# Kernel optimization log

Hardware: AMD Instinct MI355X
Metric: run time of the kernel (lower is better)

Reference implementation:

```python
import jax, jax.numpy as jnp
import numpy as np
import math

N, E = 50000, 800000
NFEAT, HID, NCLASS = 512, 96, 64
NUM_LAYERS = 8
ALPHA, THETA = 0.1, 0.5


def setup_inputs() -> dict:
    key = jax.random.key(0)
    ks = jax.random.split(key, 8)
    x = jax.random.normal(ks[0], (N, NFEAT), dtype=jnp.float32)
    # dense_to_sparse(adj_t) -> edge_index; weights are discarded by the module,
    # so propagation uses unit edge weights. We generate the edge list directly.
    edge_index = jax.random.randint(ks[1], (2, E), 0, N, dtype=jnp.int32)
    s_in = 1.0 / math.sqrt(NFEAT)
    s_hid = 1.0 / math.sqrt(HID)
    W_in = jax.random.uniform(ks[2], (NFEAT, HID), jnp.float32, -s_in, s_in)
    b_in = jax.random.uniform(ks[3], (HID,), jnp.float32, -s_in, s_in)
    conv_W = jax.random.uniform(ks[4], (NUM_LAYERS, HID, HID), jnp.float32, -s_hid, s_hid)
    W_out = jax.random.uniform(ks[5], (HID, NCLASS), jnp.float32, -s_hid, s_hid)
    b_out = jax.random.uniform(ks[6], (NCLASS,), jnp.float32, -s_hid, s_hid)
    return {"x": x, "edge_index": edge_index, "W_in": W_in, "b_in": b_in,
            "conv_W": conv_W, "W_out": W_out, "b_out": b_out}


def reference(x, edge_index, W_in, b_in, conv_W, W_out, b_out):
    # Eval mode: dropout is identity.
    src, dst = edge_index[0], edge_index[1]
    h = jax.nn.relu(x @ W_in + b_in)          # [N, HID]
    x0 = h
    for layer in range(NUM_LAYERS):
        beta = math.log(THETA / (layer + 1) + 1.0)
        # sparse propagation: out[i] = sum over edges (j -> i) of h[j]
        agg = jax.ops.segment_sum(h[src], dst, num_segments=N)   # [N, HID]
        hc = (1.0 - ALPHA) * agg + ALPHA * x0                    # initial residual
        h = jax.nn.relu((1.0 - beta) * hc + beta * (hc @ conv_W[layer]))
    out = h @ W_out + b_out                   # [N, NCLASS]
    return jax.nn.log_softmax(out, axis=-1)
```

## Files before the change

kernel.cpp:

```cpp
#include <hip/hip_runtime.h>
#include <math.h>

#define N_NODES 50000
#define N_EDGES 800000
#define NFEAT   512
#define HID     96
#define NCLASS  64
#define NUM_LAYERS 8
#define ALPHA   0.1f
#define NSB     49
#define NBB     196

typedef __attribute__((ext_vector_type(8))) short short8;
typedef __attribute__((ext_vector_type(4))) float f32x4;

__device__ __forceinline__ unsigned short f2bf(float f) {
    unsigned int u = __float_as_uint(f);
    unsigned int r = u + 0x7FFF + ((u >> 16) & 1);
    return (unsigned short)(r >> 16);
}
__device__ __forceinline__ float bflo(unsigned int u) { return __uint_as_float(u << 16); }
__device__ __forceinline__ float bfhi(unsigned int u) { return __uint_as_float(u & 0xFFFF0000u); }
__device__ __forceinline__ float bf2f(short s) {
    return __uint_as_float(((unsigned int)(unsigned short)s) << 16);
}

__global__ void hist_kernel(const int* __restrict__ dst, int* __restrict__ deg) {
    int e = blockIdx.x * blockDim.x + threadIdx.x;
    if (e < N_EDGES) atomicAdd(&deg[dst[e]], 1);
}

__global__ void scan1_kernel(const int* __restrict__ deg, int* __restrict__ row_start,
                             int* __restrict__ blk_sum) {
    __shared__ int sd[1024];
    int t = threadIdx.x;
    int i = blockIdx.x * 1024 + t;
    int v = (i < N_NODES) ? ((deg[i] + 3) & ~3) : 0;
    sd[t] = v;
    __syncthreads();
    for (int off = 1; off < 1024; off <<= 1) {
        int tv = (t >= off) ? sd[t - off] : 0;
        __syncthreads();
        sd[t] += tv;
        __syncthreads();
    }
    if (i < N_NODES) row_start[i] = sd[t] - v;
    if (t == 1023) blk_sum[blockIdx.x] = sd[1023];
}

__global__ void scan2_kernel(const int* __restrict__ blk_sum, int* __restrict__ blk_off) {
    if (threadIdx.x == 0) {
        int acc = 0;
        for (int b = 0; b < NSB; b++) { blk_off[b] = acc; acc += blk_sum[b]; }
    }
}

__global__ void scan3_kernel(int* __restrict__ row_start, const int* __restrict__ blk_off) {
    int i = blockIdx.x * 1024 + threadIdx.x;
    if (i < N_NODES) row_start[i] += blk_off[blockIdx.x];
}

__global__ void fill_kernel(const int* __restrict__ src, const int* __restrict__ dst,
                            const int* __restrict__ row_start, int* __restrict__ cursor,
                            int* __restrict__ csr_src) {
    int e = blockIdx.x * blockDim.x + threadIdx.x;
    if (e < N_EDGES) {
        int d = dst[e];
        int pos = row_start[d] + atomicAdd(&cursor[d], 1);
        csr_src[pos] = src[e];
    }
}

__global__ void pad_kernel(const int* __restrict__ deg, const int* __restrict__ row_start,
                           int* __restrict__ csr_src) {
    int n = blockIdx.x * blockDim.x + threadIdx.x;
    if (n < N_NODES) {
        int d = deg[n], pd = (d + 3) & ~3, rs = row_start[n];
        for (int p = d; p < pd; p++) csr_src[rs + p] = N_NODES;
    }
}

__global__ __launch_bounds__(256) void bin_hist2_kernel(
        const int* __restrict__ deg, int* __restrict__ node_rank,
        int* __restrict__ blk_bin_cnt) {
    __shared__ int lh[64];
    int t = threadIdx.x;
    if (t < 64) lh[t] = 0;
    __syncthreads();
    int n = blockIdx.x * 256 + t;
    if (n < N_NODES) {
        int nq = (deg[n] + 3) >> 2; if (nq > 63) nq = 63;
        node_rank[n] = atomicAdd(&lh[nq], 1);
    }
    __syncthreads();
    if (t < 64) blk_bin_cnt[blockIdx.x * 64 + t] = lh[t];
}

__global__ void bin_offsets_kernel(const int* __restrict__ blk_bin_cnt,
                                   int* __restrict__ blk_bin_off,
                                   int* __restrict__ bin_base) {
    __shared__ int tot[64];
    int b = threadIdx.x;
    int acc = 0;
    for (int blk = 0; blk < NBB; blk++) {
        blk_bin_off[blk * 64 + b] = acc;
        acc += blk_bin_cnt[blk * 64 + b];
    }
    tot[b] = acc;
    __syncthreads();
    if (b == 0) {
        int a = 0;
        for (int i = 63; i >= 0; i--) { bin_base[i] = a; a += tot[i]; }
    }
}

__global__ __launch_bounds__(256) void bin_place_kernel(
        const int* __restrict__ deg, const int* __restrict__ node_rank,
        const int* __restrict__ blk_bin_off, const int* __restrict__ bin_base,
        int* __restrict__ perm) {
    int n = blockIdx.x * 256 + threadIdx.x;
    if (n < N_NODES) {
        int nq = (deg[n] + 3) >> 2; if (nq > 63) nq = 63;
        perm[bin_base[nq] + blk_bin_off[blockIdx.x * 64 + nq] + node_rank[n]] = n;
    }
}

__global__ void zero_dummy_kernel(short* __restrict__ h0, short* __restrict__ hb,
                                  short* __restrict__ hc) {
    int t = threadIdx.x;
    if (t < HID) {
        h0[(size_t)N_NODES * HID + t] = 0;
        hb[(size_t)N_NODES * HID + t] = 0;
        hc[(size_t)N_NODES * HID + t] = 0;
    }
}

__global__ void convert_win_kernel(const float* __restrict__ W, short* __restrict__ Wt) {
    int n = blockIdx.x;
    int k = threadIdx.x;
    Wt[(size_t)n * NFEAT + k] = (short)f2bf(W[(size_t)k * HID + n]);
}

__global__ void convert_wout_kernel(const float* __restrict__ W, short* __restrict__ Wt) {
    int n = blockIdx.x;
    int k = threadIdx.x;
    Wt[(size_t)n * HID + k] = (short)f2bf(W[(size_t)k * NCLASS + n]);
}

__global__ void convert_wconv_kernel(const float* __restrict__ W, short* __restrict__ Wc) {
    int n = blockIdx.x;
    int l = blockIdx.y;
    int k = threadIdx.x;
    Wc[(size_t)l * HID * HID + (size_t)n * HID + k] =
        (short)f2bf(W[(size_t)l * HID * HID + (size_t)k * HID + n]);
}

__global__ __launch_bounds__(256) void gemm_in_kernel(
        const float* __restrict__ x, const short* __restrict__ Wt,
        const float* __restrict__ b, short* __restrict__ h0) {
    int tid  = threadIdx.x;
    int wave = tid >> 6, lane = tid & 63;
    int quad = lane >> 4, l16 = lane & 15;
    int row0 = blockIdx.x * 64 + wave * 16;
    int arow = row0 + l16; if (arow >= N_NODES) arow = N_NODES - 1;
    const float* xrow = &x[(size_t)arow * NFEAT];
    const short* wrow = &Wt[(size_t)l16 * NFEAT + quad * 8];

    f32x4 acc[6];
#pragma unroll
    for (int n = 0; n < 6; n++) acc[n] = (f32x4){0.f, 0.f, 0.f, 0.f};

#pragma unroll
    for (int k0 = 0; k0 < NFEAT; k0 += 32) {
        float4 v0 = *(const float4*)&xrow[k0 + quad * 8];
        float4 v1 = *(const float4*)&xrow[k0 + quad * 8 + 4];
        union { short8 s; uint4 u; } af;
        af.u.x = (unsigned)f2bf(v0.x) | ((unsigned)f2bf(v0.y) << 16);
        af.u.y = (unsigned)f2bf(v0.z) | ((unsigned)f2bf(v0.w) << 16);
        af.u.z = (unsigned)f2bf(v1.x) | ((unsigned)f2bf(v1.y) << 16);
        af.u.w = (unsigned)f2bf(v1.z) | ((unsigned)f2bf(v1.w) << 16);
#pragma unroll
        for (int n = 0; n < 6; n++) {
            short8 bfrag = *(const short8*)&wrow[(size_t)n * 16 * NFEAT + k0];
            acc[n] = __builtin_amdgcn_mfma_f32_16x16x32_bf16(af.s, bfrag, acc[n], 0, 0, 0);
        }
    }
#pragma unroll
    for (int n = 0; n < 6; n++) {
        int col = n * 16 + l16;
        float bias = b[col];
#pragma unroll
        for (int r = 0; r < 4; r++) {
            int grow = row0 + quad * 4 + r;
            if (grow < N_NODES) {
                float v = acc[n][r] + bias;
                v = v > 0.f ? v : 0.f;
                h0[(size_t)grow * HID + col] = (short)f2bf(v);
            }
        }
    }
}

__global__ __launch_bounds__(384) void layer_kernel(
        const short* __restrict__ h_in, const short* __restrict__ x0bf,
        const int* __restrict__ row_start, const int* __restrict__ deg,
        const int* __restrict__ csr_src, const int* __restrict__ perm,
        const short* __restrict__ Wc, float beta, short* __restrict__ h_out) {
    __shared__ short As[32][104];
    __shared__ int   snode[32];
    int tid = threadIdx.x;
    int tx = tid % 12;
    int ty = tid / 12;
    int idx = blockIdx.x * 32 + ty;
    bool valid = idx < N_NODES;
    int node = valid ? perm[idx] : (N_NODES - 1);
    if (tx == 0) snode[ty] = valid ? node : -1;

    int s = row_start[node];
    int d = deg[node];
    int nq = (d + 3) >> 2;
    const int4* c4 = (const int4*)(csr_src + s);
    float acc[8];
#pragma unroll
    for (int j = 0; j < 8; j++) acc[j] = 0.f;
    for (int i = 0; i < nq; i++) {
        int4 idxv = c4[i];
        uint4 a0 = *(const uint4*)&h_in[(size_t)idxv.x * HID + tx * 8];
        uint4 a1 = *(const uint4*)&h_in[(size_t)idxv.y * HID + tx * 8];
        uint4 a2 = *(const uint4*)&h_in[(size_t)idxv.z * HID + tx * 8];
        uint4 a3 = *(const uint4*)&h_in[(size_t)idxv.w * HID + tx * 8];
        acc[0] += bflo(a0.x) + bflo(a1.x) + bflo(a2.x) + bflo(a3.x);
        acc[1] += bfhi(a0.x) + bfhi(a1.x) + bfhi(a2.x) + bfhi(a3.x);
        acc[2] += bflo(a0.y) + bflo(a1.y) + bflo(a2.y) + bflo(a3.y);
        acc[3] += bfhi(a0.y) + bfhi(a1.y) + bfhi(a2.y) + bfhi(a3.y);
        acc[4] += bflo(a0.z) + bflo(a1.z) + bflo(a2.z) + bflo(a3.z);
        acc[5] += bfhi(a0.z) + bfhi(a1.z) + bfhi(a2.z) + bfhi(a3.z);
        acc[6] += bflo(a0.w) + bflo(a1.w) + bflo(a2.w) + bflo(a3.w);
        acc[7] += bfhi(a0.w) + bfhi(a1.w) + bfhi(a2.w) + bfhi(a3.w);
    }
    uint4 xq = *(const uint4*)&x0bf[(size_t)node * HID + tx * 8];
    float hc[8];
    hc[0] = (1.f - ALPHA) * acc[0] + ALPHA * bflo(xq.x);
    hc[1] = (1.f - ALPHA) * acc[1] + ALPHA * bfhi(xq.x);
    hc[2] = (1.f - ALPHA) * acc[2] + ALPHA * bflo(xq.y);
    hc[3] = (1.f - ALPHA) * acc[3] + ALPHA * bfhi(xq.y);
    hc[4] = (1.f - ALPHA) * acc[4] + ALPHA * bflo(xq.z);
    hc[5] = (1.f - ALPHA) * acc[5] + ALPHA * bfhi(xq.z);
    hc[6] = (1.f - ALPHA) * acc[6] + ALPHA * bflo(xq.w);
    hc[7] = (1.f - ALPHA) * acc[7] + ALPHA * bfhi(xq.w);
    {
        uint4 pk;
        pk.x = (unsigned)f2bf(hc[0]) | ((unsigned)f2bf(hc[1]) << 16);
        pk.y = (unsigned)f2bf(hc[2]) | ((unsigned)f2bf(hc[3]) << 16);
        pk.z = (unsigned)f2bf(hc[4]) | ((unsigned)f2bf(hc[5]) << 16);
        pk.w = (unsigned)f2bf(hc[6]) | ((unsigned)f2bf(hc[7]) << 16);
        *(uint4*)&As[ty][tx * 8] = pk;
    }
    __syncthreads();

    int wave = tid >> 6, lane = tid & 63;
    int quad = lane >> 4, l16 = lane & 15;
    int rt = wave & 1;
    int ct0 = (wave >> 1) * 2, ct1 = ct0 + 1;

    f32x4 g0 = (f32x4){0.f,0.f,0.f,0.f}, g1 = (f32x4){0.f,0.f,0.f,0.f};
#pragma unroll
    for (int ks = 0; ks < 3; ks++) {
        short8 afrag = *(const short8*)&As[rt * 16 + l16][ks * 32 + quad * 8];
        short8 b0 = *(const short8*)&Wc[(size_t)(ct0 * 16 + l16) * HID + ks * 32 + quad * 8];
        short8 b1 = *(const short8*)&Wc[(size_t)(ct1 * 16 + l16) * HID + ks * 32 + quad * 8];
        g0 = __builtin_amdgcn_mfma_f32_16x16x32_bf16(afrag, b0, g0, 0, 0, 0);
        g1 = __builtin_amdgcn_mfma_f32_16x16x32_bf16(afrag, b1, g1, 0, 0, 0);
    }
    float ob = 1.0f - beta;
#pragma unroll
    for (int r = 0; r < 4; r++) {
        int lrow = rt * 16 + quad * 4 + r;
        int nd = snode[lrow];
        if (nd >= 0) {
            int c0 = ct0 * 16 + l16;
            int c1 = ct1 * 16 + l16;
            float v0 = ob * bf2f(As[lrow][c0]) + beta * g0[r];
            float v1 = ob * bf2f(As[lrow][c1]) + beta * g1[r];
            v0 = v0 > 0.f ? v0 : 0.f;
            v1 = v1 > 0.f ? v1 : 0.f;
            h_out[(size_t)nd * HID + c0] = (short)f2bf(v0);
            h_out[(size_t)nd * HID + c1] = (short)f2bf(v1);
        }
    }
}

__global__ __launch_bounds__(256) void out_kernel(
        const short* __restrict__ h_bf, const short* __restrict__ Wt,
        const float* __restrict__ b, float* __restrict__ out) {
    int tid = threadIdx.x;
    int wave = tid >> 6, lane = tid & 63;
    int quad = lane >> 4, l16 = lane & 15;
    int row0 = blockIdx.x * 64 + wave * 16;

    f32x4 acc[4];
#pragma unroll
    for (int n = 0; n < 4; n++) acc[n] = (f32x4){0.f, 0.f, 0.f, 0.f};

    int arow = row0 + l16; if (arow > N_NODES) arow = N_NODES;
#pragma unroll
    for (int ks = 0; ks < 3; ks++) {
        short8 afrag = *(const short8*)&h_bf[(size_t)arow * HID + ks * 32 + quad * 8];
#pragma unroll
        for (int n = 0; n < 4; n++) {
            short8 bfrag = *(const short8*)&Wt[(size_t)(n * 16 + l16) * HID + ks * 32 + quad * 8];
            acc[n] = __builtin_amdgcn_mfma_f32_16x16x32_bf16(afrag, bfrag, acc[n], 0, 0, 0);
        }
    }
#pragma unroll
    for (int n = 0; n < 4; n++) {
        float bias = b[n * 16 + l16];
#pragma unroll
        for (int r = 0; r < 4; r++) acc[n][r] += bias;
    }
#pragma unroll
    for (int r = 0; r < 4; r++) {
        float m = acc[0][r];
        m = fmaxf(m, acc[1][r]); m = fmaxf(m, acc[2][r]); m = fmaxf(m, acc[3][r]);
#pragma unroll
        for (int off = 1; off < 16; off <<= 1) m = fmaxf(m, __shfl_xor(m, off));
        float s = __expf(acc[0][r] - m) + __expf(acc[1][r] - m)
                + __expf(acc[2][r] - m) + __expf(acc[3][r] - m);
#pragma unroll
        for (int off = 1; off < 16; off <<= 1) s += __shfl_xor(s, off);
        float lse = m + __logf(s);
        int grow = row0 + quad * 4 + r;
        if (grow < N_NODES) {
#pragma unroll
            for (int n = 0; n < 4; n++)
                out[(size_t)grow * NCLASS + n * 16 + l16] = acc[n][r] - lse;
        }
    }
}

extern "C" void kernel_launch(void* const* d_in, const int* in_sizes, int n_in,
                              void* d_out, int out_size, void* d_ws, size_t ws_size,
                              hipStream_t stream) {
    const float* x      = (const float*)d_in[0];
    const int*   ei     = (const int*)d_in[1];
    const int*   srcp   = ei;
    const int*   dstp   = ei + N_EDGES;
    const float* W_in   = (const float*)d_in[2];
    const float* b_in   = (const float*)d_in[3];
    const float* conv_W = (const float*)d_in[4];
    const float* W_out  = (const float*)d_in[5];
    const float* b_out  = (const float*)d_in[6];
    float* out = (float*)d_out;

    short* h0  = (short*)d_ws;
    short* h_b = h0  + (size_t)(N_NODES + 1) * HID;
    short* h_c = h_b + (size_t)(N_NODES + 1) * HID;
    short* Wt_in  = h_c + (size_t)(N_NODES + 1) * HID;
    short* Wt_out = Wt_in + (size_t)HID * NFEAT;
    short* Wc     = Wt_out + (size_t)NCLASS * HID;
    int* deg        = (int*)(Wc + (size_t)NUM_LAYERS * HID * HID);
    int* row_start  = deg + N_NODES;
    int* cursor     = row_start + N_NODES;
    int* blk_sum    = cursor + N_NODES;
    int* blk_off    = blk_sum + 64;
    int* bin_base   = blk_off + 64;
    int* node_rank  = bin_base + 64;
    int* perm       = node_rank + N_NODES;
    int* blk_bin_cnt= perm + N_NODES;
    int* blk_bin_off= blk_bin_cnt + NBB * 64;
    int* csr_src    = blk_bin_off + NBB * 64;

    hipMemsetAsync(deg,    0, N_NODES * sizeof(int), stream);
    hipMemsetAsync(cursor, 0, N_NODES * sizeof(int), stream);
    hist_kernel<<<(N_EDGES + 255) / 256, 256, 0, stream>>>(dstp, deg);
    scan1_kernel<<<NSB, 1024, 0, stream>>>(deg, row_start, blk_sum);
    scan2_kernel<<<1, 64, 0, stream>>>(blk_sum, blk_off);
    scan3_kernel<<<NSB, 1024, 0, stream>>>(row_start, blk_off);
    fill_kernel<<<(N_EDGES + 255) / 256, 256, 0, stream>>>(srcp, dstp, row_start, cursor, csr_src);
    pad_kernel<<<(N_NODES + 255) / 256, 256, 0, stream>>>(deg, row_start, csr_src);
    bin_hist2_kernel<<<NBB, 256, 0, stream>>>(deg, node_rank, blk_bin_cnt);
    bin_offsets_kernel<<<1, 64, 0, stream>>>(blk_bin_cnt, blk_bin_off, bin_base);
    bin_place_kernel<<<NBB, 256, 0, stream>>>(deg, node_rank, blk_bin_off, bin_base, perm);

    convert_win_kernel<<<HID, NFEAT, 0, stream>>>(W_in, Wt_in);
    convert_wout_kernel<<<NCLASS, HID, 0, stream>>>(W_out, Wt_out);
    convert_wconv_kernel<<<dim3(HID, NUM_LAYERS), HID, 0, stream>>>(conv_W, Wc);
    gemm_in_kernel<<<(N_NODES + 63) / 64, 256, 0, stream>>>(x, Wt_in, b_in, h0);
    zero_dummy_kernel<<<1, 128, 0, stream>>>(h0, h_b, h_c);

    short* cur = h0;
    short* nxt = h_b;
    for (int l = 0; l < NUM_LAYERS; l++) {
        float beta = logf(0.5f / (float)(l + 1) + 1.0f);
        layer_kernel<<<(N_NODES + 31) / 32, 384, 0, stream>>>(
            cur, h0, row_start, deg, csr_src, perm, Wc + (size_t)l * HID * HID, beta, nxt);
        cur = nxt;
        nxt = (cur == h_b) ? h_c : h_b;
    }

    out_kernel<<<(N_NODES + 63) / 64, 256, 0, stream>>>(cur, Wt_out, b_out, out);
}
```

Measured before the change: 566.4 us.

## Stage input GEMM x tiles through LDS with async global_load_lds double buffering

The input projection GEMM now streams x through a double-buffered LDS tile using global_load_lds, with an XOR swizzle to avoid bank conflicts. This lets the next K-chunk load overlap with the current chunk's MFMAs. W_in is pre-packed into the exact MFMA B-fragment order, so each lane reads one contiguous 16-byte fragment per column block. The change adds LDS use (32KB per block), which may reduce occupancy, plus a block barrier on every chunk.

```diff
diff --git a/kernel.cpp b/kernel.cpp
--- a/kernel.cpp
+++ b/kernel.cpp
@@ -23,6 +23,12 @@
 __device__ __forceinline__ float bfhi(unsigned int u) { return __uint_as_float(u & 0xFFFF0000u); }
 __device__ __forceinline__ float bf2f(short s) {
     return __uint_as_float(((unsigned int)(unsigned short)s) << 16);
+}
+
+__device__ __forceinline__ void gload16(const float* g, float* l) {
+    __builtin_amdgcn_global_load_lds(
+        (const __attribute__((address_space(1))) void*)g,
+        (__attribute__((address_space(3))) void*)l, 16, 0, 0);
 }
 
 __global__ void hist_kernel(const int* __restrict__ dst, int* __restrict__ deg) {
@@ -136,9 +142,16 @@
 }
 
 __global__ void convert_win_kernel(const float* __restrict__ W, short* __restrict__ Wt) {
-    int n = blockIdx.x;
-    int k = threadIdx.x;
-    Wt[(size_t)n * NFEAT + k] = (short)f2bf(W[(size_t)k * HID + n]);
+    int t = blockIdx.x * 256 + threadIdx.x;
+    int lane = t & 63;
+    int n    = (t >> 6) % 6;
+    int ks   = t / 384;
+    int quad = lane >> 4, l16 = lane & 15;
+    short8 v;
+#pragma unroll
+    for (int j = 0; j < 8; j++)
+        v[j] = (short)f2bf(W[(size_t)(ks * 32 + quad * 8 + j) * HID + n * 16 + l16]);
+    *(short8*)&Wt[(size_t)t * 8] = v;
 }
 
 __global__ void convert_wout_kernel(const float* __restrict__ W, short* __restrict__ Wt) {
@@ -156,42 +169,71 @@
 }
 
 __global__ __launch_bounds__(256) void gemm_in_kernel(
-        const float* __restrict__ x, const short* __restrict__ Wt,
+        const float* __restrict__ x, const short* __restrict__ WtT,
         const float* __restrict__ b, short* __restrict__ h0) {
+    __shared__ __align__(16) float As[2][4096];
     int tid  = threadIdx.x;
     int wave = tid >> 6, lane = tid & 63;
     int quad = lane >> 4, l16 = lane & 15;
-    int row0 = blockIdx.x * 64 + wave * 16;
-    int arow = row0 + l16; if (arow >= N_NODES) arow = N_NODES - 1;
-    const float* xrow = &x[(size_t)arow * NFEAT];
-    const short* wrow = &Wt[(size_t)l16 * NFEAT + quad * 8];
+    int row0 = blockIdx.x * 64;
+
+    const float* gsrc[4];
+#pragma unroll
+    for (int r = 0; r < 4; r++) {
+        int rl  = r * 4 + (lane >> 4);
+        int row = row0 + wave * 16 + rl;
+        if (row >= N_NODES) row = N_NODES - 1;
+        int c2s = (lane & 15) ^ rl;
+        gsrc[r] = &x[(size_t)row * NFEAT + c2s * 4];
+    }
 
     f32x4 acc[6];
 #pragma unroll
     for (int n = 0; n < 6; n++) acc[n] = (f32x4){0.f, 0.f, 0.f, 0.f};
 
-#pragma unroll
-    for (int k0 = 0; k0 < NFEAT; k0 += 32) {
-        float4 v0 = *(const float4*)&xrow[k0 + quad * 8];
-        float4 v1 = *(const float4*)&xrow[k0 + quad * 8 + 4];
-        union { short8 s; uint4 u; } af;
-        af.u.x = (unsigned)f2bf(v0.x) | ((unsigned)f2bf(v0.y) << 16);
-        af.u.y = (unsigned)f2bf(v0.z) | ((unsigned)f2bf(v0.w) << 16);
-        af.u.z = (unsigned)f2bf(v1.x) | ((unsigned)f2bf(v1.y) << 16);
-        af.u.w = (unsigned)f2bf(v1.z) | ((unsigned)f2bf(v1.w) << 16);
-#pragma unroll
-        for (int n = 0; n < 6; n++) {
-            short8 bfrag = *(const short8*)&wrow[(size_t)n * 16 * NFEAT + k0];
-            acc[n] = __builtin_amdgcn_mfma_f32_16x16x32_bf16(af.s, bfrag, acc[n], 0, 0, 0);
-        }
-    }
+    {
+        float* lb = &As[0][wave * 1024];
+#pragma unroll
+        for (int r = 0; r < 4; r++) gload16(gsrc[r], lb + r * 256);
+    }
+
+#pragma unroll
+    for (int c = 0; c < 8; c++) {
+        __syncthreads();
+        if (c < 7) {
+            float* nb = &As[(c + 1) & 1][wave * 1024];
+#pragma unroll
+            for (int r = 0; r < 4; r++) gload16(gsrc[r] + (c + 1) * 64, nb + r * 256);
+        }
+        const float* cb = &As[c & 1][wave * 1024 + l16 * 64];
+#pragma unroll
+        for (int s = 0; s < 2; s++) {
+            int c2a = s * 8 + quad * 2;
+            f32x4 fa = *(const f32x4*)&cb[((c2a    ) ^ l16) * 4];
+            f32x4 fb = *(const f32x4*)&cb[((c2a + 1) ^ l16) * 4];
+            union { short8 sv; uint4 u; } af;
+            af.u.x = (unsigned)f2bf(fa[0]) | ((unsigned)f2bf(fa[1]) << 16);
+            af.u.y = (unsigned)f2bf(fa[2]) | ((unsigned)f2bf(fa[3]) << 16);
+            af.u.z = (unsigned)f2bf(fb[0]) | ((unsigned)f2bf(fb[1]) << 16);
+            af.u.w = (unsigned)f2bf(fb[2]) | ((unsigned)f2bf(fb[3]) << 16);
+            int ks = c * 2 + s;
+            const short* bbase = &WtT[(size_t)(ks * 6) * 512 + lane * 8];
+#pragma unroll
+            for (int n = 0; n < 6; n++) {
+                short8 bfrag = *(const short8*)&bbase[n * 512];
+                acc[n] = __builtin_amdgcn_mfma_f32_16x16x32_bf16(af.sv, bfrag, acc[n], 0, 0, 0);
+            }
+        }
+    }
+
+    int row0w = row0 + wave * 16;
 #pragma unroll
     for (int n = 0; n < 6; n++) {
         int col = n * 16 + l16;
         float bias = b[col];
 #pragma unroll
         for (int r = 0; r < 4; r++) {
-            int grow = row0 + quad * 4 + r;
+            int grow = row0w + quad * 4 + r;
             if (grow < N_NODES) {
                 float v = acc[n][r] + bias;
                 v = v > 0.f ? v : 0.f;
@@ -382,7 +424,7 @@
     bin_offsets_kernel<<<1, 64, 0, stream>>>(blk_bin_cnt, blk_bin_off, bin_base);
     bin_place_kernel<<<NBB, 256, 0, stream>>>(deg, node_rank, blk_bin_off, bin_base, perm);
 
-    convert_win_kernel<<<HID, NFEAT, 0, stream>>>(W_in, Wt_in);
+    convert_win_kernel<<<24, 256, 0, stream>>>(W_in, Wt_in);
     convert_wout_kernel<<<NCLASS, HID, 0, stream>>>(W_out, Wt_out);
     convert_wconv_kernel<<<dim3(HID, NUM_LAYERS), HID, 0, stream>>>(conv_W, Wc);
     gemm_in_kernel<<<(N_NODES + 63) / 64, 256, 0, stream>>>(x, Wt_in, b_in, h0);
```

Result: faster. 538.1 us (-5.0%).
